# Kernel optimization log

Hardware: AMD Instinct MI355X
Metric: run time of the kernel (lower is better)

## Reference

```python
import jax, jax.numpy as jnp
import numpy as np

DIM = 768
HEADS = 12
HEAD_DIM = DIM // HEADS
R = 8            # LoRA rank (cfg.EXPERT_LOW_RANK)
E = 4            # number of routed LoRA experts in proj (cfg.EXPERT_NUM)
LORA_SCALE = 1.0 / R   # lora_alpha(=1) / r
TOPK_T_PCT = 50  # cfg.topk_tempalte (percent)
TOPK_S_PCT = 25  # cfg.topk_search (percent)
B = 4
N_M = 256        # template / memory tokens
N_S = 1024       # search tokens
N = N_M + N_S
MEM = 1280       # cached memory kv length


def setup_inputs() -> dict:
    key = jax.random.key(0)
    ks = jax.random.split(key, 24)
    g = lambda i, shape: jax.random.normal(ks[i], shape, dtype=jnp.float32) * 0.02
    return dict(
        x=jax.random.normal(ks[0], (B, N, DIM), dtype=jnp.float32),
        id_total=jax.random.normal(ks[1], (B, N_M, DIM), dtype=jnp.float32),
        mem_k=jax.random.normal(ks[2], (B, HEADS, MEM, HEAD_DIM), dtype=jnp.float32),
        mem_v=jax.random.normal(ks[3], (B, HEADS, MEM, HEAD_DIM), dtype=jnp.float32),
        W_qkv=g(4, (3 * DIM, DIM)), b_qkv=g(5, (3 * DIM,)),
        qkv_A=g(6, (3, R, DIM)), qkv_B=g(7, (3, DIM, R)),
        W_proj=g(8, (DIM, DIM)), b_proj=g(9, (DIM,)),
        route_W=g(10, (E, DIM)), proj_A=g(11, (E, R, DIM)), proj_B=g(12, (E, DIM, R)),
        W_idk=g(13, (HEADS, DIM)), b_idk=g(14, (HEADS,)),
        idk_A=g(15, (R, DIM)), idk_B=g(16, (HEADS, R)),
        W_idv=g(17, (DIM, DIM)), b_idv=g(18, (DIM,)),
        idv_A=g(19, (R, DIM)), idv_B=g(20, (DIM, R)),
    )


def _lora1(x, W, b, A, Bm):
    # LinearExperts with lora_num=1: softmax over a single route logit == 1.0
    return x @ W.T + b + ((x @ A.T) @ Bm.T) * LORA_SCALE


def _softmax_w_top(att, top):
    # topk values (sorted desc) -> stable exp relative to the max -> normalize -> scatter
    vals, idx = jax.lax.top_k(att, top)
    e = jnp.exp(vals - vals[..., :1])
    e = e / jnp.sum(e, axis=-1, keepdims=True)
    b, h, q, _ = att.shape
    bi = jnp.arange(b)[:, None, None, None]
    hi = jnp.arange(h)[None, :, None, None]
    qi = jnp.arange(q)[None, None, :, None]
    return jnp.zeros_like(att).at[bi, hi, qi, idx].set(e.astype(att.dtype))


def _forward(x, id_total, mem_k, mem_v, W_qkv, b_qkv, qkv_A, qkv_B,
             W_proj, b_proj, route_W, proj_A, proj_B,
             W_idk, b_idk, idk_A, idk_B, W_idv, b_idv, idv_A, idv_B):
    Bb, Nn, C = x.shape
    Nm = id_total.shape[1]
    Ns = Nn - Nm
    H, D = HEADS, C // HEADS
    # MergedLinear qkv: dense + per-group (q,k,v) LoRA
    low = jnp.einsum('bnc,grc->bngr', x, qkv_A)
    lora = (jnp.einsum('bngr,gcr->bngc', low, qkv_B) * LORA_SCALE).reshape(Bb, Nn, 3 * C)
    qkv = (x @ W_qkv.T + b_qkv + lora).reshape(Bb, Nn, 3, H, D).transpose(2, 0, 3, 1, 4)
    q, k, v = qkv[0], qkv[1], qkv[2]          # each (B,H,N,D)
    k_m, v_m, v_s = k[:, :, :Nm], v[:, :, :Nm], v[:, :, Nm:]
    # memory-token ID gating (id_add=True path)
    ID_K = _lora1(id_total, W_idk, b_idk, idk_A, idk_B)   # (B,Nm,H)
    ID_V = _lora1(id_total, W_idv, b_idv, idv_A, idv_B)   # (B,Nm,C)
    k_m_id = k_m * (1.0 + jnp.tanh(ID_K)).transpose(0, 2, 1)[..., None]
    v_m_flat = v_m.transpose(0, 2, 1, 3).reshape(Bb, Nm, C) + ID_V
    v_m_id = v_m_flat.reshape(Bb, Nm, H, D).transpose(0, 2, 1, 3)
    v_add_id = jnp.concatenate([v_m_id, v_s], axis=2)
    q = q * (D ** -0.5)
    q_m, q_s = q[:, :, :Nm], q[:, :, Nm:]
    # template self-attention with topk softmax
    attn_m = q_m @ k_m_id.transpose(0, 1, 3, 2)           # (B,H,Nm,Nm)
    attn_m = _softmax_w_top(attn_m, int(TOPK_T_PCT / 100 * Nm))
    x_m = (attn_m @ v_m_id).transpose(0, 2, 1, 3).reshape(Bb, Nm, C)
    # search attention over [mem_k, k] (k is the ORIGINAL un-gated key, as in torch)
    k_full = jnp.concatenate([mem_k, k], axis=2)
    v_full = jnp.concatenate([mem_v, v_add_id], axis=2)
    attn_s = q_s @ k_full.transpose(0, 1, 3, 2)           # (B,H,Ns,MEM+N)
    attn_s = _softmax_w_top(attn_s, int(TOPK_S_PCT / 100 * k_full.shape[2]))
    x_s = (attn_s @ v_full).transpose(0, 2, 1, 3).reshape(Bb, Ns, C)
    xo = jnp.concatenate([x_m, x_s], axis=1)
    # LinearExperts proj: dense + softmax-routed LoRA experts
    route = jax.nn.softmax((xo @ route_W.T).astype(jnp.float32), axis=-1).astype(xo.dtype)
    low = jnp.einsum('bnc,erc->bner', xo, proj_A)
    up = jnp.einsum('bner,ecr->bnec', low, proj_B)
    out = xo @ W_proj.T + b_proj + jnp.einsum('bne,bnec->bnc', route, up) * LORA_SCALE
    return out, k_m_id, v_m_id


def reference(x, id_total, mem_k, mem_v, W_qkv, b_qkv, qkv_A, qkv_B,
              W_proj, b_proj, route_W, proj_A, proj_B,
              W_idk, b_idk, idk_A, idk_B, W_idv, b_idv, idv_A, idv_B):
    return _forward(x, id_total, mem_k, mem_v, W_qkv, b_qkv, qkv_A, qkv_B,
                    W_proj, b_proj, route_W, proj_A, proj_B,
                    W_idk, b_idk, idk_A, idk_B, W_idv, b_idv, idv_A, idv_B)
```

## Files before the change

### kernel.cpp

```cpp
#include <hip/hip_runtime.h>
#include <cstddef>

#define Bq    4
#define Hh    12
#define Dd    64
#define NNtok 1280
#define DIMc  768
#define KAUG  800
#define NBH   48

typedef __attribute__((ext_vector_type(8))) short bf16x8;
typedef __attribute__((ext_vector_type(4))) float f32x4;

static const size_t OVb   = 0;
static const size_t OXO   = 3932160;
static const size_t OQL   = 7864320;
static const size_t OIDK  = 7987200;
static const size_t OIDV  = 7999488;
static const size_t OLK   = 8785920;
static const size_t OLV   = 8794112;
static const size_t OQH   = 8986624;
static const size_t OKFH  = 10952704;
static const size_t OVTH  = 14884864;
static const size_t OKMH  = 18817024;
static const size_t OVMTH = 19210240;
static const size_t OAa   = 19603456;
static const size_t OWa   = 21651456;
static const size_t OWa2  = 22573056;

static const size_t KMID_OFF = 3932160;
static const size_t VMID_OFF = 4718592;

__device__ __forceinline__ unsigned int pk_bf16(float a, float b) {
  unsigned int ua = __float_as_uint(a), ub = __float_as_uint(b);
  ua += 0x7fffu + ((ua >> 16) & 1u);
  ub += 0x7fffu + ((ub >> 16) & 1u);
  return (ua >> 16) | (ub & 0xffff0000u);
}
__device__ __forceinline__ unsigned short bf16_1(float a) {
  unsigned int ua = __float_as_uint(a);
  ua += 0x7fffu + ((ua >> 16) & 1u);
  return (unsigned short)(ua >> 16);
}
__device__ __forceinline__ float bf2f(unsigned int h) {
  return __uint_as_float(h << 16);
}

__global__ __launch_bounds__(256) void prep(
    const float* __restrict__ mem_k, const float* __restrict__ mem_v,
    const float* __restrict__ W_qkv, const float* __restrict__ qkvB,
    const float* __restrict__ W_proj, const float* __restrict__ projB,
    unsigned short* __restrict__ kfh, unsigned short* __restrict__ vth,
    unsigned short* __restrict__ Wa, unsigned short* __restrict__ Wa2,
    const float* __restrict__ x, const float* __restrict__ qkvA,
    float* __restrict__ qlow,
    const float* __restrict__ id_tot, const float* __restrict__ idkA,
    const float* __restrict__ idvA, float* __restrict__ lowk,
    float* __restrict__ lowv)
{
  __shared__ float tl[64][65];
  const int blk = blockIdx.x, t = threadIdx.x;
  if (blk < 1920) {
    size_t idx = ((size_t)blk * 256 + t) * 8;
    int bh = (int)(idx / 81920);
    int r  = (int)(idx % 81920);
    const float* s = mem_k + (size_t)bh * 81920 + r;
    float4 a = *(const float4*)s;
    float4 b = *(const float4*)(s + 4);
    unsigned int* dp = (unsigned int*)(kfh + (size_t)bh * 163840 + r);
    dp[0] = pk_bf16(a.x, a.y); dp[1] = pk_bf16(a.z, a.w);
    dp[2] = pk_bf16(b.x, b.y); dp[3] = pk_bf16(b.z, b.w);
  } else if (blk < 2880) {
    int b2 = blk - 1920;
    int bh = b2 / 20, t0 = (b2 % 20) * 64;
    const float* sb = mem_v + (size_t)bh * 81920 + (size_t)t0 * 64;
#pragma unroll
    for (int p = 0; p < 4; ++p) {
      int flat = p * 256 + t;
      int r = flat >> 4, c4 = (flat & 15) << 2;
      float4 v = *(const float4*)(sb + r * 64 + c4);
      tl[r][c4 + 0] = v.x; tl[r][c4 + 1] = v.y;
      tl[r][c4 + 2] = v.z; tl[r][c4 + 3] = v.w;
    }
    __syncthreads();
    unsigned short* db = vth + (size_t)bh * 163840 + t0;
#pragma unroll
    for (int p = 0; p < 8; ++p) {
      int flat = p * 256 + t;
      int d = flat >> 5, u = flat & 31;
      *(unsigned int*)(db + (size_t)d * 2560 + 2 * u) = pk_bf16(tl[2 * u][d], tl[2 * u + 1][d]);
    }
  } else if (blk < 6480) {
    int idx = (blk - 2880) * 256 + t;
    int row = idx / 400, c = (idx % 400) * 2;
    float a, b;
    if (c < 768) {
      a = W_qkv[(size_t)row * 768 + c]; b = W_qkv[(size_t)row * 768 + c + 1];
    } else {
      int g = row / 768, jj = row % 768;
      int e0 = c - 768, e1 = e0 + 1;
      a = (e0 < 24 && (e0 >> 3) == g) ? qkvB[(size_t)g * 6144 + jj * 8 + (e0 & 7)] * 0.125f : 0.f;
      b = (e1 < 24 && (e1 >> 3) == g) ? qkvB[(size_t)g * 6144 + jj * 8 + (e1 & 7)] * 0.125f : 0.f;
    }
    *(unsigned int*)(Wa + (size_t)row * KAUG + c) = pk_bf16(a, b);
  } else if (blk < 7680) {
    int idx = (blk - 6480) * 256 + t;
    int row = idx / 400, c = (idx % 400) * 2;
    float a, b;
    if (c < 768) {
      a = W_proj[(size_t)row * 768 + c]; b = W_proj[(size_t)row * 768 + c + 1];
    } else {
      int e0 = c - 768, e1 = e0 + 1;
      a = projB[(size_t)(e0 >> 3) * 6144 + row * 8 + (e0 & 7)];
      b = projB[(size_t)(e1 >> 3) * 6144 + row * 8 + (e1 & 7)];
    }
    *(unsigned int*)(Wa2 + (size_t)row * KAUG + c) = pk_bf16(a, b);
  } else {
    const int wv = t >> 6, ln = t & 63;
    int b2 = blk - 7680;
    if (b2 < 1280) {
      size_t row = (size_t)b2 * 4 + wv;
      const float* s = x + row * DIMc;
      float xr[12];
#pragma unroll
      for (int i = 0; i < 12; ++i) xr[i] = s[ln + i * 64];
      float p[24];
#pragma unroll
      for (int o = 0; o < 24; ++o) {
        const float* m = qkvA + (size_t)o * DIMc;
        float acc = 0.f;
#pragma unroll
        for (int i = 0; i < 12; ++i) acc += xr[i] * m[ln + i * 64];
        p[o] = acc;
      }
#pragma unroll
      for (int off = 32; off; off >>= 1)
#pragma unroll
        for (int o = 0; o < 24; ++o) p[o] += __shfl_xor(p[o], off, 64);
      if (ln == 0) {
#pragma unroll
        for (int o = 0; o < 24; ++o) qlow[row * 24 + o] = p[o];
      }
    } else {
      size_t row = (size_t)(b2 - 1280) * 4 + wv;
      const float* s = id_tot + row * DIMc;
      float xr[12];
#pragma unroll
      for (int i = 0; i < 12; ++i) xr[i] = s[ln + i * 64];
      float p[16];
#pragma unroll
      for (int o = 0; o < 8; ++o) {
        const float* m1 = idkA + (size_t)o * DIMc;
        const float* m2 = idvA + (size_t)o * DIMc;
        float a1 = 0.f, a2 = 0.f;
#pragma unroll
        for (int i = 0; i < 12; ++i) {
          a1 += xr[i] * m1[ln + i * 64];
          a2 += xr[i] * m2[ln + i * 64];
        }
        p[o] = a1; p[8 + o] = a2;
      }
#pragma unroll
      for (int off = 32; off; off >>= 1)
#pragma unroll
        for (int o = 0; o < 16; ++o) p[o] += __shfl_xor(p[o], off, 64);
      if (ln == 0) {
#pragma unroll
        for (int o = 0; o < 8; ++o) { lowk[row * 8 + o] = p[o]; lowv[row * 8 + o] = p[8 + o]; }
      }
    }
  }
}

__global__ __launch_bounds__(256) void idv_idk(
    const float* __restrict__ id_tot,
    const float* __restrict__ W_idv, const float* __restrict__ b_idv,
    const float* __restrict__ lowv, const float* __restrict__ idv_B,
    float* __restrict__ IDV,
    const float* __restrict__ W_idk, const float* __restrict__ b_idk,
    const float* __restrict__ lowk, const float* __restrict__ idk_B,
    float* __restrict__ IDK)
{
  __shared__ alignas(16) float As[16][68];
  __shared__ alignas(16) float Bs[16][68];
  const int blk = blockIdx.x, t = threadIdx.x;
  if (blk < 192) {
    const int tx = t & 15, ty = t >> 4;
    const int bn = (blk % 12) * 64, bm = (blk / 12) * 64;
    const int am = t >> 2, ak = (t & 3) << 2;
    float acc[4][4] = {};
    for (int k0 = 0; k0 < 768; k0 += 16) {
      float4 av = *(const float4*)(id_tot + (size_t)(bm + am) * 768 + k0 + ak);
      float4 bv = *(const float4*)(W_idv + (size_t)(bn + am) * 768 + k0 + ak);
      As[ak + 0][am] = av.x; As[ak + 1][am] = av.y; As[ak + 2][am] = av.z; As[ak + 3][am] = av.w;
      Bs[ak + 0][am] = bv.x; Bs[ak + 1][am] = bv.y; Bs[ak + 2][am] = bv.z; Bs[ak + 3][am] = bv.w;
      __syncthreads();
#pragma unroll
      for (int kk = 0; kk < 16; ++kk) {
        float4 a4 = *(const float4*)&As[kk][ty << 2];
        float4 b4 = *(const float4*)&Bs[kk][tx << 2];
        float ar[4] = { a4.x, a4.y, a4.z, a4.w };
        float br[4] = { b4.x, b4.y, b4.z, b4.w };
#pragma unroll
        for (int i = 0; i < 4; ++i)
#pragma unroll
          for (int j = 0; j < 4; ++j) acc[i][j] += ar[i] * br[j];
      }
      __syncthreads();
    }
#pragma unroll
    for (int i = 0; i < 4; ++i) {
      int mg = bm + (ty << 2) + i;
#pragma unroll
      for (int j = 0; j < 4; ++j) {
        int col = bn + (tx << 2) + j;
        float v = acc[i][j] + b_idv[col];
        float lo = 0.f;
#pragma unroll
        for (int r = 0; r < 8; ++r) lo += lowv[(size_t)mg * 8 + r] * idv_B[(size_t)col * 8 + r];
        IDV[(size_t)mg * 768 + col] = v + lo * 0.125f;
      }
    }
  } else {
    int wv = t >> 6, ln = t & 63;
    size_t row = (size_t)(blk - 192) * 4 + wv;
    const float* s = id_tot + row * DIMc;
    float xr[12];
#pragma unroll
    for (int i = 0; i < 12; ++i) xr[i] = s[ln + i * 64];
    float p[12];
#pragma unroll
    for (int h = 0; h < 12; ++h) {
      const float* m = W_idk + (size_t)h * DIMc;
      float acc = 0.f;
#pragma unroll
      for (int i = 0; i < 12; ++i) acc += xr[i] * m[ln + i * 64];
      p[h] = acc;
    }
#pragma unroll
    for (int off = 32; off; off >>= 1)
#pragma unroll
      for (int h = 0; h < 12; ++h) p[h] += __shfl_xor(p[h], off, 64);
    if (ln == 0) {
#pragma unroll
      for (int h = 0; h < 12; ++h) {
        float lo = 0.f;
#pragma unroll
        for (int r = 0; r < 8; ++r) lo += lowk[row * 8 + r] * idk_B[h * 8 + r];
        IDK[row * Hh + h] = 1.f + tanhf(p[h] + b_idk[h] + lo * 0.125f);
      }
    }
  }
}

__global__ __launch_bounds__(256) void fixup_kernel(
    float* __restrict__ vb, const float* __restrict__ IDK,
    const float* __restrict__ IDV, float* __restrict__ kmid,
    float* __restrict__ vmid, unsigned short* __restrict__ kmh)
{
  int e = blockIdx.x * 256 + threadIdx.x;
  int d  = e & 63;
  int r1 = e >> 6;
  int tt = r1 & 255;
  int r2 = r1 >> 8;
  int h  = r2 % Hh;
  int b  = r2 / Hh;
  float km = kmid[e] * IDK[(size_t)(b * 256 + tt) * Hh + h];
  kmid[e] = km;
  kmh[e] = bf16_1(km);
  size_t src = ((size_t)(b * Hh + h) * NNtok + tt) * Dd + d;
  float vv = vb[src] + IDV[(size_t)(b * 256 + tt) * DIMc + h * 64 + d];
  vb[src] = vv;
  vmid[e] = vv;
}

__global__ __launch_bounds__(256) void transpose_post(
    const float* __restrict__ vb, unsigned short* __restrict__ vth,
    unsigned short* __restrict__ vmth)
{
  __shared__ float tl[64][65];
  const int blk = blockIdx.x, t = threadIdx.x;
  int bh, t0, dstCols, colOfs;
  unsigned short* dstp;
  size_t dstBh;
  if (blk < 960) { bh = blk / 20; t0 = (blk % 20) * 64; dstp = vth; dstBh = 163840; dstCols = 2560; colOfs = 1280; }
  else { int b2 = blk - 960; bh = b2 / 4; t0 = (b2 % 4) * 64; dstp = vmth; dstBh = 16384; dstCols = 256; colOfs = 0; }
  const float* sb = vb + (size_t)bh * 81920 + (size_t)t0 * 64;
#pragma unroll
  for (int p = 0; p < 4; ++p) {
    int flat = p * 256 + t;
    int r = flat >> 4, c4 = (flat & 15) << 2;
    float4 v = *(const float4*)(sb + r * 64 + c4);
    tl[r][c4 + 0] = v.x; tl[r][c4 + 1] = v.y;
    tl[r][c4 + 2] = v.z; tl[r][c4 + 3] = v.w;
  }
  __syncthreads();
  unsigned short* db = dstp + (size_t)bh * dstBh + colOfs + t0;
#pragma unroll
  for (int p = 0; p < 8; ++p) {
    int flat = p * 256 + t;
    int d = flat >> 5, u = flat & 31;
    *(unsigned int*)(db + (size_t)d * dstCols + 2 * u) = pk_bf16(tl[2 * u][d], tl[2 * u + 1][d]);
  }
}

__global__ __launch_bounds__(256) void cast_pack(
    const float* __restrict__ mainp, const float* __restrict__ extra,
    unsigned short* __restrict__ dst, int extraN)
{
  int idx = blockIdx.x * 256 + threadIdx.x;
  int row = idx / 100, c8 = (idx % 100) * 8;
  unsigned int w[4];
  if (c8 < 768) {
    const float* s = mainp + (size_t)row * 768 + c8;
    float4 a = *(const float4*)s;
    float4 b = *(const float4*)(s + 4);
    w[0] = pk_bf16(a.x, a.y); w[1] = pk_bf16(a.z, a.w);
    w[2] = pk_bf16(b.x, b.y); w[3] = pk_bf16(b.z, b.w);
  } else {
    float v[8];
#pragma unroll
    for (int j = 0; j < 8; ++j) {
      int e = c8 - 768 + j;
      v[j] = (e < extraN) ? extra[(size_t)row * extraN + e] : 0.f;
    }
    w[0] = pk_bf16(v[0], v[1]); w[1] = pk_bf16(v[2], v[3]);
    w[2] = pk_bf16(v[4], v[5]); w[3] = pk_bf16(v[6], v[7]);
  }
  *(uint4*)(dst + (size_t)row * KAUG + c8) = make_uint4(w[0], w[1], w[2], w[3]);
}

__global__ __launch_bounds__(256) void cast_pack_proj(
    const float* __restrict__ xo, const float* __restrict__ routeW,
    const float* __restrict__ projA, unsigned short* __restrict__ dst)
{
  const int wv = threadIdx.x >> 6, ln = threadIdx.x & 63;
  size_t row = (size_t)blockIdx.x * 4 + wv;
  const float* s = xo + row * DIMc;
  float xr[12];
#pragma unroll
  for (int i = 0; i < 12; ++i) xr[i] = s[ln + i * 64];
  float pr[4];
#pragma unroll
  for (int o = 0; o < 4; ++o) {
    const float* m = routeW + (size_t)o * DIMc;
    float acc = 0.f;
#pragma unroll
    for (int i = 0; i < 12; ++i) acc += xr[i] * m[ln + i * 64];
    pr[o] = acc;
  }
  float pl[32];
#pragma unroll
  for (int o = 0; o < 32; ++o) {
    const float* m = projA + (size_t)o * DIMc;
    float acc = 0.f;
#pragma unroll
    for (int i = 0; i < 12; ++i) acc += xr[i] * m[ln + i * 64];
    pl[o] = acc;
  }
#pragma unroll
  for (int off = 32; off; off >>= 1) {
#pragma unroll
    for (int o = 0; o < 4; ++o) pr[o] += __shfl_xor(pr[o], off, 64);
#pragma unroll
    for (int o = 0; o < 32; ++o) pl[o] += __shfl_xor(pl[o], off, 64);
  }
  float mx = fmaxf(fmaxf(pr[0], pr[1]), fmaxf(pr[2], pr[3]));
  float e0 = __expf(pr[0] - mx), e1 = __expf(pr[1] - mx),
        e2 = __expf(pr[2] - mx), e3 = __expf(pr[3] - mx);
  float inv = 0.125f / (e0 + e1 + e2 + e3);
  float rt[4] = { e0 * inv, e1 * inv, e2 * inv, e3 * inv };
  unsigned short* drow = dst + row * KAUG;
  for (int g = ln; g < 100; g += 64) {
    int c8 = g * 8;
    unsigned int w[4];
    if (c8 < 768) {
      const float* p = s + c8;
      float4 a = *(const float4*)p;
      float4 b = *(const float4*)(p + 4);
      w[0] = pk_bf16(a.x, a.y); w[1] = pk_bf16(a.z, a.w);
      w[2] = pk_bf16(b.x, b.y); w[3] = pk_bf16(b.z, b.w);
    } else {
      float v[8];
#pragma unroll
      for (int j = 0; j < 8; ++j) {
        int e = c8 - 768 + j;
        v[j] = (e < 32) ? rt[e >> 3] * pl[e] : 0.f;
      }
      w[0] = pk_bf16(v[0], v[1]); w[1] = pk_bf16(v[2], v[3]);
      w[2] = pk_bf16(v[4], v[5]); w[3] = pk_bf16(v[6], v[7]);
    }
    *(uint4*)(drow + c8) = make_uint4(w[0], w[1], w[2], w[3]);
  }
}

__global__ __launch_bounds__(256) void gemm_mfma(
    const unsigned short* __restrict__ A, const unsigned short* __restrict__ W,
    const float* __restrict__ bias, int mode, float* __restrict__ dst,
    unsigned short* __restrict__ qh, float* __restrict__ kmid,
    float* __restrict__ vb, unsigned short* __restrict__ kfh)
{
  const int t = threadIdx.x, w = t >> 6, l = t & 63;
  const int m = l & 15, quad = l >> 4;
  const int bm = blockIdx.y * 128 + (w >> 1) * 64;
  const int bn = blockIdx.x * 128 + (w & 1) * 64;
  f32x4 acc[4][4] = {};
  const unsigned short* Ab = A + (size_t)(bm + m) * KAUG;
  const unsigned short* Wb = W + (size_t)(bn + m) * KAUG;
  for (int kk = 0; kk < KAUG; kk += 32) {
    bf16x8 af[4], bf[4];
#pragma unroll
    for (int i = 0; i < 4; ++i) af[i] = *(const bf16x8*)(Ab + (size_t)i * 16 * KAUG + kk + quad * 8);
#pragma unroll
    for (int j = 0; j < 4; ++j) bf[j] = *(const bf16x8*)(Wb + (size_t)j * 16 * KAUG + kk + quad * 8);
#pragma unroll
    for (int i = 0; i < 4; ++i)
#pragma unroll
      for (int j = 0; j < 4; ++j)
        acc[i][j] = __builtin_amdgcn_mfma_f32_16x16x32_bf16(af[i], bf[j], acc[i][j], 0, 0, 0);
  }

  float bj[4];
#pragma unroll
  for (int j = 0; j < 4; ++j) bj[j] = bias[bn + j * 16 + m];

  if (mode == 2) {
#pragma unroll
    for (int i = 0; i < 4; ++i)
#pragma unroll
      for (int r = 0; r < 4; ++r) {
        int row = bm + i * 16 + quad * 4 + r;
#pragma unroll
        for (int j = 0; j < 4; ++j)
          dst[(size_t)row * 768 + bn + j * 16 + m] = acc[i][j][r] + bj[j];
      }
    return;
  }
  int g = (blockIdx.x * 128) / DIMc;
#pragma unroll
  for (int j = 0; j < 4; ++j) {
    int col = bn + j * 16 + m;
    int jj = col - g * DIMc, hh = jj >> 6, d = jj & 63;
#pragma unroll
    for (int i = 0; i < 4; ++i)
#pragma unroll
      for (int r = 0; r < 4; ++r) {
        int row = bm + i * 16 + quad * 4 + r;
        int bb = row / NNtok, tt = row % NNtok;
        float v = acc[i][j][r] + bj[j];
        if (g == 0) {
          qh[((size_t)(bb * Hh + hh) * NNtok + tt) * Dd + d] = bf16_1(v * 0.125f);
        } else if (g == 1) {
          kfh[((size_t)(bb * Hh + hh) * 2560 + 1280 + tt) * Dd + d] = bf16_1(v);
          if (tt < 256) kmid[((size_t)(bb * Hh + hh) * 256 + tt) * Dd + d] = v;
        } else {
          vb[((size_t)(bb * Hh + hh) * NNtok + tt) * Dd + d] = v;
        }
      }
  }
}

__device__ __forceinline__ void radix_sel(
    unsigned int* hist, int l, int& kk, int& ceq, unsigned int& bin)
{
  unsigned int h0 = hist[4 * l + 0], h1 = hist[4 * l + 1],
               h2 = hist[4 * l + 2], h3 = hist[4 * l + 3];
  unsigned int s3 = h3, s2 = h2 + s3, s1 = h1 + s2, s0 = h0 + s1;
  unsigned int tsum = s0;
#pragma unroll
  for (int off = 1; off < 64; off <<= 1) {
    unsigned int other = __shfl(tsum, l + off, 64);
    tsum += (l + off < 64) ? other : 0u;
  }
  unsigned int T = tsum - s0;
  unsigned int Sv0 = T + s0, Sv1 = T + s1, Sv2 = T + s2, Sv3 = T + s3, Sv4 = T;
  int fb = -1, fkk = 0, fceq = 0;
  unsigned int ukk = (unsigned int)kk;
  if (Sv0 >= ukk && Sv1 < ukk) { fb = 4 * l + 0; fkk = (int)(ukk - Sv1); fceq = (int)(Sv0 - Sv1); }
  if (Sv1 >= ukk && Sv2 < ukk) { fb = 4 * l + 1; fkk = (int)(ukk - Sv2); fceq = (int)(Sv1 - Sv2); }
  if (Sv2 >= ukk && Sv3 < ukk) { fb = 4 * l + 2; fkk = (int)(ukk - Sv3); fceq = (int)(Sv2 - Sv3); }
  if (Sv3 >= ukk && Sv4 < ukk) { fb = 4 * l + 3; fkk = (int)(ukk - Sv4); fceq = (int)(Sv3 - Sv4); }
  unsigned long long mb = __ballot(fb >= 0);
  int src = __ffsll(mb) - 1;
  bin = (unsigned int)__shfl(fb, src, 64);
  kk  = __shfl(fkk, src, 64);
  ceq = __shfl(fceq, src, 64);
}

template<int NK>
__device__ __forceinline__ void attn_body(
    int blk,
    const unsigned short* __restrict__ qh,
    const unsigned short* __restrict__ kf,
    const unsigned short* __restrict__ vt,
    int TK, int qrow0, float* __restrict__ xo, int nofs,
    unsigned short* __restrict__ scb, unsigned int* __restrict__ histb,
    float* __restrict__ wavemaxb, float* __restrict__ rowinv)
{
  constexpr int SCP = NK + 8;
  constexpr int W = NK / 128;
  constexpr int NRB = (NK == 256) ? 32 : 128;

  const int t = threadIdx.x, w = t >> 6, l = t & 63;
  const int xcd  = blk & 7;
  const int slot = blk >> 3;
  const int bh   = xcd * (NBH / 8) + slot / NRB;
  const int rb   = slot % NRB;
  const int b = bh / Hh, h = bh % Hh;
  const int qbase = qrow0 + rb * 8;
  const int m = l & 15, quad = l >> 4;

  bf16x8 aq0 = {0,0,0,0,0,0,0,0}, aq1 = {0,0,0,0,0,0,0,0};
  if (m < 8) {
    const unsigned short* qp = qh + ((size_t)bh * NNtok + qbase + m) * Dd + quad * 8;
    aq0 = *(const bf16x8*)qp;
    aq1 = *(const bf16x8*)(qp + 32);
  }
  float mx[4] = { -3.0e38f, -3.0e38f, -3.0e38f, -3.0e38f };
  constexpr int ITA = NK / 64;
  constexpr int GA = (ITA >= 4) ? 4 : ITA;
  const unsigned short* kpA = kf + (size_t)bh * NK * Dd + (size_t)(w * 16 + m) * Dd + quad * 8;
  bf16x8 kbuf[2][GA][2];
#pragma unroll
  for (int i = 0; i < GA; ++i) {
    kbuf[0][i][0] = *(const bf16x8*)(kpA + (size_t)i * 64 * Dd);
    kbuf[0][i][1] = *(const bf16x8*)(kpA + (size_t)i * 64 * Dd + 32);
  }
  int ab = 0;
  for (int g0 = 0; g0 < ITA; g0 += GA) {
    if (g0 + GA < ITA) {
#pragma unroll
      for (int i = 0; i < GA; ++i) {
        kbuf[1 - ab][i][0] = *(const bf16x8*)(kpA + (size_t)(g0 + GA + i) * 64 * Dd);
        kbuf[1 - ab][i][1] = *(const bf16x8*)(kpA + (size_t)(g0 + GA + i) * 64 * Dd + 32);
      }
    }
#pragma unroll
    for (int i = 0; i < GA; ++i) {
      int n0 = w * 16 + (g0 + i) * 64;
      f32x4 acc = {0.f, 0.f, 0.f, 0.f};
      acc = __builtin_amdgcn_mfma_f32_16x16x32_bf16(aq0, kbuf[ab][i][0], acc, 0, 0, 0);
      acc = __builtin_amdgcn_mfma_f32_16x16x32_bf16(aq1, kbuf[ab][i][1], acc, 0, 0, 0);
      if (quad < 2) {
#pragma unroll
        for (int r = 0; r < 4; ++r) {
          float v = acc[r];
          mx[r] = fmaxf(mx[r], v);
          scb[(quad * 4 + r) * SCP + n0 + m] = bf16_1(v);
        }
      }
    }
    ab ^= 1;
  }
#pragma unroll
  for (int off = 1; off < 16; off <<= 1)
#pragma unroll
    for (int r = 0; r < 4; ++r) mx[r] = fmaxf(mx[r], __shfl_xor(mx[r], off, 64));
  if (l == 0) {
#pragma unroll
    for (int r = 0; r < 4; ++r) wavemaxb[w * 8 + r] = mx[r];
  }
  if (l == 16) {
#pragma unroll
    for (int r = 0; r < 4; ++r) wavemaxb[w * 8 + 4 + r] = mx[r];
  }
  __syncthreads();

  const int r0i = w * 2, r1i = w * 2 + 1;
  unsigned int* sp0 = (unsigned int*)(scb + r0i * SCP);
  unsigned int* sp1 = (unsigned int*)(scb + r1i * SCP);
  unsigned int* h0 = histb + r0i * 256;
  unsigned int* h1 = histb + r1i * 256;
#pragma unroll
  for (int z = 0; z < 4; ++z) { h0[l + z * 64] = 0u; h1[l + z * 64] = 0u; }
  unsigned int kw0[W], kw1[W];
#pragma unroll
  for (int j = 0; j < W; ++j) {
    unsigned int v0 = sp0[j * 64 + l];
    unsigned int v1 = sp1[j * 64 + l];
    v0 = v0 ^ (((v0 >> 15) & 0x00010001u) * 0x7fffu + 0x80008000u);
    v1 = v1 ^ (((v1 >> 15) & 0x00010001u) * 0x7fffu + 0x80008000u);
    kw0[j] = v0; kw1[j] = v1;
    atomicAdd(&h0[(v0 >> 8) & 255u], 1u);
    atomicAdd(&h0[v0 >> 24], 1u);
    atomicAdd(&h1[(v1 >> 8) & 255u], 1u);
    atomicAdd(&h1[v1 >> 24], 1u);
  }
  int kk0 = TK, kk1 = TK;
  int ceq0s, ceq1s;
  unsigned int bin0, bin1;
  radix_sel(h0, l, kk0, ceq0s, bin0);
  radix_sel(h1, l, kk1, ceq1s, bin1);
  const unsigned int pf0 = bin0 << 8, pf1 = bin1 << 8;
  (void)ceq0s; (void)ceq1s;

  auto finish = [&](unsigned int* kwp, unsigned int prefix, int kk, int row,
                    unsigned int* sp) {
    unsigned int* hist = histb + row * 256;
#pragma unroll
    for (int z = 0; z < 4; ++z) hist[l + z * 64] = 0u;
    const unsigned int pfx8 = prefix >> 8;
#pragma unroll
    for (int j = 0; j < W; ++j) {
      unsigned int k2 = kwp[j];
      unsigned int lo = k2 & 0xFFFFu, hi = k2 >> 16;
      if ((lo >> 8) == pfx8) atomicAdd(&hist[lo & 255u], 1u);
      if ((hi >> 8) == pfx8) atomicAdd(&hist[hi & 255u], 1u);
    }
    unsigned int b2;
    int ceq = 0;
    radix_sel(hist, l, kk, ceq, b2);
    const unsigned int Tkey = prefix | b2;
    const int need = kk;
    if (need < ceq) {
      int seen = 0;
      unsigned long long below = (1ull << l) - 1ull;
#pragma unroll
      for (int j = 0; j < W; ++j) {
        unsigned int k2 = kwp[j];
        bool eq0 = ((k2 & 0xFFFFu) == Tkey);
        bool eq1 = ((k2 >> 16) == Tkey);
        unsigned long long m0 = __ballot(eq0), m1 = __ballot(eq1);
        int bfr = __popcll(m0 & below) + __popcll(m1 & below);
        if (eq0 && (seen + bfr) >= need) kwp[j] &= 0xFFFF0000u;
        if (eq1 && (seen + bfr + (eq0 ? 1 : 0)) >= need) kwp[j] &= 0x0000FFFFu;
        seen += __popcll(m0) + __popcll(m1);
      }
    }
    float rm = fmaxf(fmaxf(wavemaxb[0 * 8 + row], wavemaxb[1 * 8 + row]),
                     fmaxf(wavemaxb[2 * 8 + row], wavemaxb[3 * 8 + row]));
    float sum = 0.f;
#pragma unroll
    for (int j = 0; j < W; ++j) {
      unsigned int k2 = kwp[j];
      unsigned int lo = k2 & 0xFFFFu, hi = k2 >> 16;
      unsigned int mm = ((~k2 >> 15) & 0x00010001u) * 0x7fffu + 0x80008000u;
      unsigned int o2 = k2 ^ mm;
      float v0 = bf2f(o2 & 0xFFFFu);
      float v1 = bf2f(o2 >> 16);
      float w0 = (lo >= Tkey) ? __expf(v0 - rm) : 0.f;
      float w1 = (hi >= Tkey) ? __expf(v1 - rm) : 0.f;
      sp[j * 64 + l] = pk_bf16(w0, w1);
      sum += w0 + w1;
    }
#pragma unroll
    for (int off = 32; off; off >>= 1) sum += __shfl_xor(sum, off, 64);
    if (l == 0) rowinv[row] = 1.f / sum;
  };
  finish(kw0, pf0, kk0, r0i, sp0);
  finish(kw1, pf1, kk1, r1i, sp1);
  __syncthreads();

  constexpr int ITD = NK / 32;
  constexpr int GD = (ITD >= 4) ? 4 : ITD;
  const unsigned short* vrow = vt + (size_t)bh * Dd * NK + (size_t)(w * 16 + m) * NK + quad * 8;
  f32x4 o = {0.f, 0.f, 0.f, 0.f};
  const bf16x8 zz = {0,0,0,0,0,0,0,0};
  bf16x8 vbuf[2][GD], wbuf[2][GD];
#pragma unroll
  for (int i = 0; i < GD; ++i) {
    vbuf[0][i] = *(const bf16x8*)(vrow + i * 32);
    wbuf[0][i] = (m < 8) ? *(const bf16x8*)(scb + m * SCP + i * 32 + quad * 8) : zz;
  }
  int db = 0;
  for (int g0 = 0; g0 < ITD; g0 += GD) {
    if (g0 + GD < ITD) {
#pragma unroll
      for (int i = 0; i < GD; ++i) {
        vbuf[1 - db][i] = *(const bf16x8*)(vrow + (g0 + GD + i) * 32);
        wbuf[1 - db][i] = (m < 8) ? *(const bf16x8*)(scb + m * SCP + (g0 + GD + i) * 32 + quad * 8) : zz;
      }
    }
#pragma unroll
    for (int i = 0; i < GD; ++i)
      o = __builtin_amdgcn_mfma_f32_16x16x32_bf16(wbuf[db][i], vbuf[db][i], o, 0, 0, 0);
    db ^= 1;
  }
  if (quad < 2) {
#pragma unroll
    for (int r = 0; r < 4; ++r) {
      int row = quad * 4 + r;
      int n = nofs + rb * 8 + row;
      xo[((size_t)b * NNtok + n) * DIMc + h * 64 + w * 16 + m] = o[r] * rowinv[row];
    }
  }
}

__global__ __launch_bounds__(256, 3) void attn_fused(
    const unsigned short* __restrict__ qh,
    const unsigned short* __restrict__ kfh, const unsigned short* __restrict__ vth,
    const unsigned short* __restrict__ kmh, const unsigned short* __restrict__ vmth,
    float* __restrict__ xo)
{
  __shared__ alignas(16) unsigned short sc_raw[8 * 2568];
  __shared__ unsigned int hist_raw[8 * 256];
  __shared__ float wm_raw[32];
  __shared__ float ri_raw[8];
  if (blockIdx.x < 6144) {
    attn_body<2560>((int)blockIdx.x, qh, kfh, vth, 640, 256, xo, 256,
                    sc_raw, hist_raw, wm_raw, ri_raw);
  } else {
    attn_body<256>((int)blockIdx.x - 6144, qh, kmh, vmth, 128, 0, xo, 0,
                   sc_raw, hist_raw, wm_raw, ri_raw);
  }
}

extern "C" void kernel_launch(void* const* d_in, const int* in_sizes, int n_in,
                              void* d_out, int out_size, void* d_ws, size_t ws_size,
                              hipStream_t stream)
{
  const float* x       = (const float*)d_in[0];
  const float* id_tot  = (const float*)d_in[1];
  const float* mem_k   = (const float*)d_in[2];
  const float* mem_v   = (const float*)d_in[3];
  const float* W_qkv   = (const float*)d_in[4];
  const float* b_qkv   = (const float*)d_in[5];
  const float* qkv_A   = (const float*)d_in[6];
  const float* qkv_B   = (const float*)d_in[7];
  const float* W_proj  = (const float*)d_in[8];
  const float* b_proj  = (const float*)d_in[9];
  const float* route_W = (const float*)d_in[10];
  const float* proj_A  = (const float*)d_in[11];
  const float* proj_B  = (const float*)d_in[12];
  const float* W_idk   = (const float*)d_in[13];
  const float* b_idk   = (const float*)d_in[14];
  const float* idk_A   = (const float*)d_in[15];
  const float* idk_B   = (const float*)d_in[16];
  const float* W_idv   = (const float*)d_in[17];
  const float* b_idv   = (const float*)d_in[18];
  const float* idv_A   = (const float*)d_in[19];
  const float* idv_B   = (const float*)d_in[20];

  float* ws   = (float*)d_ws;
  float* vb   = ws + OVb;
  float* xo   = ws + OXO;
  float* qlow = ws + OQL;
  float* IDK  = ws + OIDK;
  float* IDV  = ws + OIDV;
  float* lowk = ws + OLK;
  float* lowv = ws + OLV;
  unsigned short* qh   = (unsigned short*)(ws + OQH);
  unsigned short* kfh  = (unsigned short*)(ws + OKFH);
  unsigned short* vth  = (unsigned short*)(ws + OVTH);
  unsigned short* kmh  = (unsigned short*)(ws + OKMH);
  unsigned short* vmth = (unsigned short*)(ws + OVMTH);
  unsigned short* Aa   = (unsigned short*)(ws + OAa);
  unsigned short* Wa   = (unsigned short*)(ws + OWa);
  unsigned short* Wa2  = (unsigned short*)(ws + OWa2);

  float* out  = (float*)d_out;
  float* kmid = out + KMID_OFF;
  float* vmid = out + VMID_OFF;

  prep<<<9216, 256, 0, stream>>>(mem_k, mem_v, W_qkv, qkv_B, W_proj, proj_B,
                                 kfh, vth, Wa, Wa2,
                                 x, qkv_A, qlow, id_tot, idk_A, idv_A, lowk, lowv);

  cast_pack<<<2000, 256, 0, stream>>>(x, qlow, Aa, 24);
  gemm_mfma<<<dim3(18, 40), 256, 0, stream>>>(Aa, Wa, b_qkv, 0, nullptr,
                                              qh, kmid, vb, kfh);
  idv_idk<<<448, 256, 0, stream>>>(id_tot, W_idv, b_idv, lowv, idv_B, IDV,
                                   W_idk, b_idk, lowk, idk_B, IDK);
  fixup_kernel<<<3072, 256, 0, stream>>>(vb, IDK, IDV, kmid, vmid, kmh);

  transpose_post<<<1152, 256, 0, stream>>>(vb, vth, vmth);

  attn_fused<<<7680, 256, 0, stream>>>(qh, kfh, vth, kmh, vmth, xo);

  cast_pack_proj<<<1280, 256, 0, stream>>>(xo, route_W, proj_A, Aa);
  gemm_mfma<<<dim3(6, 40), 256, 0, stream>>>(Aa, Wa2, b_proj, 2, out,
                                             nullptr, nullptr, nullptr, nullptr);
}
```

Measured before the change: 812.3 us.

## Merge id projections with input cast and fold fixup into QKV GEMM epilogue

The idv/idk projection kernel and the x/qlow bf16 cast-pack now run as one launch, with the cast handled by the extra blocks. Because IDK and IDV are now ready before the QKV GEMM, the GEMM epilogue applies the IDK scaling to memory keys and adds IDV to memory values directly. This removes the separate fixup kernel and its read-modify-write pass over vb and kmid. In exchange the GEMM epilogue does extra gathers, and the id GEMM blocks share one launch with the many cast blocks.

```diff
diff --git a/kernel.cpp b/kernel.cpp
--- a/kernel.cpp
+++ b/kernel.cpp
@@ -172,14 +172,16 @@
   }
 }
 
-__global__ __launch_bounds__(256) void idv_idk(
+__global__ __launch_bounds__(256) void idv_idk_cast(
     const float* __restrict__ id_tot,
     const float* __restrict__ W_idv, const float* __restrict__ b_idv,
     const float* __restrict__ lowv, const float* __restrict__ idv_B,
     float* __restrict__ IDV,
     const float* __restrict__ W_idk, const float* __restrict__ b_idk,
     const float* __restrict__ lowk, const float* __restrict__ idk_B,
-    float* __restrict__ IDK)
+    float* __restrict__ IDK,
+    const float* __restrict__ x, const float* __restrict__ qlow,
+    unsigned short* __restrict__ Aa)
 {
   __shared__ alignas(16) float As[16][68];
   __shared__ alignas(16) float Bs[16][68];
@@ -221,7 +223,7 @@
         IDV[(size_t)mg * 768 + col] = v + lo * 0.125f;
       }
     }
-  } else {
+  } else if (blk < 448) {
     int wv = t >> 6, ln = t & 63;
     size_t row = (size_t)(blk - 192) * 4 + wv;
     const float* s = id_tot + row * DIMc;
@@ -250,28 +252,28 @@
         IDK[row * Hh + h] = 1.f + tanhf(p[h] + b_idk[h] + lo * 0.125f);
       }
     }
-  }
-}
-
-__global__ __launch_bounds__(256) void fixup_kernel(
-    float* __restrict__ vb, const float* __restrict__ IDK,
-    const float* __restrict__ IDV, float* __restrict__ kmid,
-    float* __restrict__ vmid, unsigned short* __restrict__ kmh)
-{
-  int e = blockIdx.x * 256 + threadIdx.x;
-  int d  = e & 63;
-  int r1 = e >> 6;
-  int tt = r1 & 255;
-  int r2 = r1 >> 8;
-  int h  = r2 % Hh;
-  int b  = r2 / Hh;
-  float km = kmid[e] * IDK[(size_t)(b * 256 + tt) * Hh + h];
-  kmid[e] = km;
-  kmh[e] = bf16_1(km);
-  size_t src = ((size_t)(b * Hh + h) * NNtok + tt) * Dd + d;
-  float vv = vb[src] + IDV[(size_t)(b * 256 + tt) * DIMc + h * 64 + d];
-  vb[src] = vv;
-  vmid[e] = vv;
+  } else {
+    int idx = (blk - 448) * 256 + t;
+    int row = idx / 100, c8 = (idx % 100) * 8;
+    unsigned int w[4];
+    if (c8 < 768) {
+      const float* s = x + (size_t)row * 768 + c8;
+      float4 a = *(const float4*)s;
+      float4 b = *(const float4*)(s + 4);
+      w[0] = pk_bf16(a.x, a.y); w[1] = pk_bf16(a.z, a.w);
+      w[2] = pk_bf16(b.x, b.y); w[3] = pk_bf16(b.z, b.w);
+    } else {
+      float v[8];
+#pragma unroll
+      for (int j = 0; j < 8; ++j) {
+        int e = c8 - 768 + j;
+        v[j] = (e < 24) ? qlow[(size_t)row * 24 + e] : 0.f;
+      }
+      w[0] = pk_bf16(v[0], v[1]); w[1] = pk_bf16(v[2], v[3]);
+      w[2] = pk_bf16(v[4], v[5]); w[3] = pk_bf16(v[6], v[7]);
+    }
+    *(uint4*)(Aa + (size_t)row * KAUG + c8) = make_uint4(w[0], w[1], w[2], w[3]);
+  }
 }
 
 __global__ __launch_bounds__(256) void transpose_post(
@@ -302,32 +304,6 @@
     int d = flat >> 5, u = flat & 31;
     *(unsigned int*)(db + (size_t)d * dstCols + 2 * u) = pk_bf16(tl[2 * u][d], tl[2 * u + 1][d]);
   }
-}
-
-__global__ __launch_bounds__(256) void cast_pack(
-    const float* __restrict__ mainp, const float* __restrict__ extra,
-    unsigned short* __restrict__ dst, int extraN)
-{
-  int idx = blockIdx.x * 256 + threadIdx.x;
-  int row = idx / 100, c8 = (idx % 100) * 8;
-  unsigned int w[4];
-  if (c8 < 768) {
-    const float* s = mainp + (size_t)row * 768 + c8;
-    float4 a = *(const float4*)s;
-    float4 b = *(const float4*)(s + 4);
-    w[0] = pk_bf16(a.x, a.y); w[1] = pk_bf16(a.z, a.w);
-    w[2] = pk_bf16(b.x, b.y); w[3] = pk_bf16(b.z, b.w);
-  } else {
-    float v[8];
-#pragma unroll
-    for (int j = 0; j < 8; ++j) {
-      int e = c8 - 768 + j;
-      v[j] = (e < extraN) ? extra[(size_t)row * extraN + e] : 0.f;
-    }
-    w[0] = pk_bf16(v[0], v[1]); w[1] = pk_bf16(v[2], v[3]);
-    w[2] = pk_bf16(v[4], v[5]); w[3] = pk_bf16(v[6], v[7]);
-  }
-  *(uint4*)(dst + (size_t)row * KAUG + c8) = make_uint4(w[0], w[1], w[2], w[3]);
 }
 
 __global__ __launch_bounds__(256) void cast_pack_proj(
@@ -398,7 +374,9 @@
     const unsigned short* __restrict__ A, const unsigned short* __restrict__ W,
     const float* __restrict__ bias, int mode, float* __restrict__ dst,
     unsigned short* __restrict__ qh, float* __restrict__ kmid,
-    float* __restrict__ vb, unsigned short* __restrict__ kfh)
+    float* __restrict__ vb, unsigned short* __restrict__ kfh,
+    const float* __restrict__ IDK, const float* __restrict__ IDV,
+    float* __restrict__ vmid, unsigned short* __restrict__ kmh)
 {
   const int t = threadIdx.x, w = t >> 6, l = t & 63;
   const int m = l & 15, quad = l >> 4;
@@ -452,9 +430,21 @@
           qh[((size_t)(bb * Hh + hh) * NNtok + tt) * Dd + d] = bf16_1(v * 0.125f);
         } else if (g == 1) {
           kfh[((size_t)(bb * Hh + hh) * 2560 + 1280 + tt) * Dd + d] = bf16_1(v);
-          if (tt < 256) kmid[((size_t)(bb * Hh + hh) * 256 + tt) * Dd + d] = v;
+          if (tt < 256) {
+            float km = v * IDK[(size_t)(bb * 256 + tt) * Hh + hh];
+            size_t e = ((size_t)(bb * Hh + hh) * 256 + tt) * Dd + d;
+            kmid[e] = km;
+            kmh[e] = bf16_1(km);
+          }
         } else {
-          vb[((size_t)(bb * Hh + hh) * NNtok + tt) * Dd + d] = v;
+          size_t src = ((size_t)(bb * Hh + hh) * NNtok + tt) * Dd + d;
+          if (tt < 256) {
+            float vv = v + IDV[(size_t)(bb * 256 + tt) * DIMc + jj];
+            vb[src] = vv;
+            vmid[((size_t)(bb * Hh + hh) * 256 + tt) * Dd + d] = vv;
+          } else {
+            vb[src] = v;
+          }
         }
       }
   }
@@ -756,12 +746,13 @@
                                  kfh, vth, Wa, Wa2,
                                  x, qkv_A, qlow, id_tot, idk_A, idv_A, lowk, lowv);
 
-  cast_pack<<<2000, 256, 0, stream>>>(x, qlow, Aa, 24);
+  idv_idk_cast<<<2448, 256, 0, stream>>>(id_tot, W_idv, b_idv, lowv, idv_B, IDV,
+                                         W_idk, b_idk, lowk, idk_B, IDK,
+                                         x, qlow, Aa);
+
   gemm_mfma<<<dim3(18, 40), 256, 0, stream>>>(Aa, Wa, b_qkv, 0, nullptr,
-                                              qh, kmid, vb, kfh);
-  idv_idk<<<448, 256, 0, stream>>>(id_tot, W_idv, b_idv, lowv, idv_B, IDV,
-                                   W_idk, b_idk, lowk, idk_B, IDK);
-  fixup_kernel<<<3072, 256, 0, stream>>>(vb, IDK, IDV, kmid, vmid, kmh);
+                                              qh, kmid, vb, kfh,
+                                              IDK, IDV, vmid, kmh);
 
   transpose_post<<<1152, 256, 0, stream>>>(vb, vth, vmth);
 
@@ -769,5 +760,6 @@
 
   cast_pack_proj<<<1280, 256, 0, stream>>>(xo, route_W, proj_A, Aa);
   gemm_mfma<<<dim3(6, 40), 256, 0, stream>>>(Aa, Wa2, b_proj, 2, out,
+                                             nullptr, nullptr, nullptr, nullptr,
                                              nullptr, nullptr, nullptr, nullptr);
 }
```

Result: no change. 816.6 us (+0.5%).
